# Optimization experiments

Hardware: AMD Instinct MI355X
Metric: run time of the kernel (lower is better)

The kernel has to match this reference:

```python
import jax, jax.numpy as jnp
import numpy as np

B = 128          # number of trees
DEPTH = 8        # complete binary tree depth -> 2^8-1 nodes per tree
NPT = 2 ** DEPTH - 1          # 255 nodes per tree
N = B * NPT                   # 32640 total nodes
E_T = NPT - 1                 # 254 edges per tree
F_IN = 64
H = 256


def _build_trees():
    """Complete binary trees; children of local node i are 2i+1, 2i+2."""
    idx = np.arange(NPT)
    depth = np.floor(np.log2(idx + 1)).astype(np.int64)
    order = (DEPTH - 1) - depth                 # leaves=0, root=DEPTH-1
    internal = idx[: NPT // 2]                  # nodes that have children
    parents = np.repeat(internal, 2)
    children = np.empty_like(parents)
    children[0::2] = 2 * internal + 1
    children[1::2] = 2 * internal + 2
    adj_local = np.stack([parents, children], axis=1)        # [E_T, 2]
    offs = (np.arange(B) * NPT)[:, None, None]
    adjacency = (adj_local[None, :, :] + offs).reshape(-1, 2)  # [B*E_T, 2]
    node_order = np.tile(order, B)                             # [N]
    edge_order = np.tile(order[parents], B)                    # [B*E_T]
    return node_order, adjacency, edge_order


def setup_inputs() -> dict:
    key = jax.random.key(0)
    ks = jax.random.split(key, 8)
    node_order, adjacency_list, edge_order = _build_trees()
    s = lambda k, shape, fan: jax.random.normal(k, shape, jnp.float32) * (fan ** -0.5)
    return {
        "features": jax.random.normal(ks[0], (N, F_IN), jnp.float32),
        "node_order": jnp.asarray(node_order, jnp.int32),
        "adjacency_list": jnp.asarray(adjacency_list, jnp.int32),
        "edge_order": jnp.asarray(edge_order, jnp.int32),
        "W_iou_w": s(ks[1], (3 * H, F_IN), F_IN),
        "W_iou_b": jnp.zeros((3 * H,), jnp.float32),
        "U_iou_w": s(ks[2], (3 * H, H), H),
        "W_f_w": s(ks[3], (H, F_IN), F_IN),
        "W_f_b": jnp.zeros((H,), jnp.float32),
        "U_f_w": s(ks[4], (H, H), H),
        "lin0_w": s(ks[5], (H, H), H),
        "lin0_b": jnp.zeros((H,), jnp.float32),
        "lin1_w": s(ks[6], (1, H), H),
        "lin1_b": jnp.zeros((1,), jnp.float32),
    }


def reference(features, node_order, adjacency_list, edge_order,
              W_iou_w, W_iou_b, U_iou_w, W_f_w, W_f_b, U_f_w,
              lin0_w, lin0_b, lin1_w, lin1_b):
    n = features.shape[0]
    parent = adjacency_list[:, 0]
    child = adjacency_list[:, 1]
    # input->gate projections, computed once for all nodes
    wx_iou = features @ W_iou_w.T + W_iou_b      # [N, 3H]
    wx_f = features @ W_f_w.T + W_f_b            # [N, H]
    h = jnp.zeros((n, H), features.dtype)
    c = jnp.zeros((n, H), features.dtype)
    # sequential bottom-up sweep over topological levels (static DEPTH levels)
    for t in range(DEPTH):
        nmask = (node_order == t)[:, None]
        emask = (edge_order == t).astype(features.dtype)[:, None]
        child_h = h[child]                       # [E, H] gather
        h_sum = jax.ops.segment_sum(child_h * emask, parent, num_segments=n)
        iou = wx_iou + h_sum @ U_iou_w.T         # [N, 3H]; h_sum==0 at level 0
        i, o, u = jnp.split(iou, 3, axis=1)
        i = jax.nn.sigmoid(i); o = jax.nn.sigmoid(o); u = jnp.tanh(u)
        f = jax.nn.sigmoid(wx_f[parent] + child_h @ U_f_w.T)  # [E, H]
        c_sum = jax.ops.segment_sum(f * c[child] * emask, parent, num_segments=n)
        new_c = i * u + c_sum
        new_h = o * jnp.tanh(new_c)
        h = jnp.where(nmask, new_h, h)
        c = jnp.where(nmask, new_c, c)
    # unbatch + mean-pool per tree (use_root=False); equal-size trees -> reshape
    x = h.reshape(B, NPT, H).mean(axis=1)        # [B, H]
    # MLP head: Linear -> ReLU -> (dropout inactive in eval) -> Linear
    x = x @ lin0_w.T + lin0_b
    x = jax.nn.relu(x)
    x = x @ lin1_w.T + lin1_b                    # [B, 1]
    return x.reshape(-1)                         # flattened, aux output is None
```

## Files before the change

### kernel.cpp

```cpp
#include <hip/hip_runtime.h>

#define B_TREES 128
#define NPT 255
#define NTOT (B_TREES * NPT)
#define FIN 64
#define HH 256

typedef short bf16x8 __attribute__((ext_vector_type(8)));
typedef float f32x4  __attribute__((ext_vector_type(4)));
typedef unsigned short u16;

__device__ __forceinline__ float sigf(float x) {
    return __frcp_rn(1.0f + __expf(-x));
}
__device__ __forceinline__ float tanh_fast(float x) {
    return __builtin_fmaf(2.0f, sigf(2.0f * x), -1.0f);
}
__device__ __forceinline__ u16 bf_hi(float v) {
    unsigned u = __float_as_uint(v);
    return (u16)((u + 0x7FFFu + ((u >> 16) & 1u)) >> 16);
}
__device__ __forceinline__ float bf_f(u16 b) { return __uint_as_float(((unsigned)b) << 16); }

__global__ __launch_bounds__(256) void pack_B(
    const float* __restrict__ Uiou, const float* __restrict__ Uf,
    const float* __restrict__ Wiou, const float* __restrict__ Wf,
    u16* __restrict__ Bhi, u16* __restrict__ Blo)
{
    int idx = blockIdx.x * 256 + threadIdx.x;
    int j    = idx & 7;
    int lane = (idx >> 3) & 63;
    int ksl  = (idx >> 9) % 10;
    int ct   = idx / 5120;
    int s = ct % 5, hb = ct / 5;
    int n = lane & 15, q = lane >> 4;
    int jH = hb * 16 + n;
    int k = (s < 4 ? ksl * 32 : 320 + ksl * 32) + q * 8 + j;

    float v = 0.0f;
    if (s == 4) {
        if (k < 576) v = Uf[(size_t)jH * HH + (k - 320)];
    } else {
        if (k < 256) {
            v = (s < 3) ? Uiou[(size_t)(s * 256 + jH) * HH + k]
                        : Uf[(size_t)jH * HH + k];
        } else {
            int kw = k - 256;
            v = (s < 3) ? Wiou[(size_t)(s * 256 + jH) * FIN + kw]
                        : 2.0f * Wf[(size_t)jH * FIN + kw];
        }
    }
    u16 hi = bf_hi(v);
    u16 lo = bf_hi(v - bf_f(hi));
    Bhi[idx] = hi;
    Blo[idx] = lo;
}

template<int NCT, bool LEAF>
__global__ __launch_bounds__(256, 2) void level_mfma(
    const float* __restrict__ feat,
    const u16* __restrict__ Bhi, const u16* __restrict__ Blo,
    const float* __restrict__ biou, const float* __restrict__ bfv,
    float* __restrict__ h, float* __restrict__ c,
    int Lt, int lg)
{
    constexpr int CSPLIT = 20 / NCT;
    constexpr int SUBS = NCT / 5;
    __shared__ char smem[73728];
    short* Ahi = (short*)smem;
    short* Alo = (short*)(smem + 36864);

    const int tid = threadIdx.x;
    const int lane = tid & 63, w = tid >> 6;
    const int cs = blockIdx.x % CSPLIT;
    const int rb = blockIdx.x / CSPLIT;
    const int m0 = rb * 32;
    const int msk = (1 << lg) - 1;
    const int ctbase = cs * 4 * NCT + w * NCT;

    const float4* Hf4 = (const float4*)h;
    const float4* Ff4 = (const float4*)feat;

    if constexpr (!LEAF) {
        for (int rep = 0; rep < 8; ++rep) {
            int flat = rep * 256 + tid;
            int m = flat >> 6, f4 = flat & 63;
            int mg = m0 + m;
            int b = mg >> lg, ii = Lt + (mg & msk);
            int gc = b * NPT + 2 * ii + 1;
            float4 h1 = Hf4[(size_t)gc * 64 + f4];
            float4 h2 = Hf4[(size_t)(gc + 1) * 64 + f4];
            float hsv[4] = {h1.x + h2.x, h1.y + h2.y, h1.z + h2.z, h1.w + h2.w};
            float hdv[4] = {h1.x - h2.x, h1.y - h2.y, h1.z - h2.z, h1.w - h2.w};
            int rt = m >> 4, lm = m & 15;
            int ks = f4 >> 3;
            int lane_ = lm + 16 * ((f4 >> 1) & 3);
            int j0 = (f4 & 1) * 4;
            ushort4 sh, sl, dh, dl;
            u16* shp = (u16*)&sh; u16* slp = (u16*)&sl;
            u16* dhp = (u16*)&dh; u16* dlp = (u16*)&dl;
#pragma unroll
            for (int e = 0; e < 4; ++e) {
                u16 a = bf_hi(hsv[e]); shp[e] = a; slp[e] = bf_hi(hsv[e] - bf_f(a));
                u16 d = bf_hi(hdv[e]); dhp[e] = d; dlp[e] = bf_hi(hdv[e] - bf_f(d));
            }
            int base_s = ((rt * 18 + ks) * 64 + lane_) * 8 + j0;
            int base_d = ((rt * 18 + ks + 10) * 64 + lane_) * 8 + j0;
            *(ushort4*)&Ahi[base_s] = sh;  *(ushort4*)&Alo[base_s] = sl;
            *(ushort4*)&Ahi[base_d] = dh;  *(ushort4*)&Alo[base_d] = dl;
        }
    }
    for (int rep = 0; rep < 2; ++rep) {
        int flat = rep * 256 + tid;
        int m = flat >> 4, f4 = flat & 15;
        int mg = m0 + m;
        int b = mg >> lg, ii = Lt + (mg & msk);
        int g = b * NPT + ii;
        float4 x4 = Ff4[(size_t)g * 16 + f4];
        float xv[4] = {x4.x, x4.y, x4.z, x4.w};
        int rt = m >> 4, lm = m & 15;
        int ks = 8 + (f4 >> 3);
        int lane_ = lm + 16 * ((f4 >> 1) & 3);
        int j0 = (f4 & 1) * 4;
        ushort4 xh, xl;
        u16* xhp = (u16*)&xh; u16* xlp = (u16*)&xl;
#pragma unroll
        for (int e = 0; e < 4; ++e) {
            u16 a = bf_hi(xv[e]); xhp[e] = a; xlp[e] = bf_hi(xv[e] - bf_f(a));
        }
        int base = ((rt * 18 + ks) * 64 + lane_) * 8 + j0;
        *(ushort4*)&Ahi[base] = xh;  *(ushort4*)&Alo[base] = xl;
    }
    __syncthreads();

    f32x4 acc[2][NCT];
#pragma unroll
    for (int rt = 0; rt < 2; ++rt)
#pragma unroll
        for (int i = 0; i < NCT; ++i) acc[rt][i] = (f32x4){0.f, 0.f, 0.f, 0.f};

    const int G0 = LEAF ? 8 : 0;
    for (int G = G0; G < 10; ++G) {
        bf16x8 ah[2], al[2];
#pragma unroll
        for (int rt = 0; rt < 2; ++rt) {
            ah[rt] = *(const bf16x8*)&Ahi[((rt * 18 + G) * 64 + lane) * 8];
            al[rt] = *(const bf16x8*)&Alo[((rt * 18 + G) * 64 + lane) * 8];
        }
#pragma unroll
        for (int ctl = 0; ctl < NCT; ++ctl) {
            if (ctl % 5 == 4) continue;
            size_t slot = (size_t)((ctbase + ctl) * 10 + G) * 512 + lane * 8;
            bf16x8 bh = *(const bf16x8*)(Bhi + slot);
            bf16x8 bl = *(const bf16x8*)(Blo + slot);
#pragma unroll
            for (int rt = 0; rt < 2; ++rt) {
                acc[rt][ctl] = __builtin_amdgcn_mfma_f32_16x16x32_bf16(ah[rt], bh, acc[rt][ctl], 0, 0, 0);
                acc[rt][ctl] = __builtin_amdgcn_mfma_f32_16x16x32_bf16(ah[rt], bl, acc[rt][ctl], 0, 0, 0);
                acc[rt][ctl] = __builtin_amdgcn_mfma_f32_16x16x32_bf16(al[rt], bh, acc[rt][ctl], 0, 0, 0);
            }
        }
    }
    if constexpr (!LEAF) {
        for (int G = 10; G < 18; ++G) {
            bf16x8 ah[2], al[2];
#pragma unroll
            for (int rt = 0; rt < 2; ++rt) {
                ah[rt] = *(const bf16x8*)&Ahi[((rt * 18 + G) * 64 + lane) * 8];
                al[rt] = *(const bf16x8*)&Alo[((rt * 18 + G) * 64 + lane) * 8];
            }
#pragma unroll
            for (int ctl = 4; ctl < NCT; ctl += 5) {
                size_t slot = (size_t)((ctbase + ctl) * 10 + (G - 10)) * 512 + lane * 8;
                bf16x8 bh = *(const bf16x8*)(Bhi + slot);
                bf16x8 bl = *(const bf16x8*)(Blo + slot);
#pragma unroll
                for (int rt = 0; rt < 2; ++rt) {
                    acc[rt][ctl] = __builtin_amdgcn_mfma_f32_16x16x32_bf16(ah[rt], bh, acc[rt][ctl], 0, 0, 0);
                    acc[rt][ctl] = __builtin_amdgcn_mfma_f32_16x16x32_bf16(ah[rt], bl, acc[rt][ctl], 0, 0, 0);
                    acc[rt][ctl] = __builtin_amdgcn_mfma_f32_16x16x32_bf16(al[rt], bh, acc[rt][ctl], 0, 0, 0);
                }
            }
        }
    }
    __syncthreads();

    float* sc = (float*)smem + w * 2592;
    const int n = lane & 15, q = lane >> 4;
#pragma unroll
    for (int sub = 0; sub < SUBS; ++sub) {
#pragma unroll
        for (int rt = 0; rt < 2; ++rt)
#pragma unroll
            for (int s = 0; s < 5; ++s) {
                f32x4 v = acc[rt][sub * 5 + s];
#pragma unroll
                for (int r = 0; r < 4; ++r)
                    sc[(rt * 16 + q * 4 + r) * 81 + s * 16 + n] = v[r];
            }
        int hb_abs = ctbase / 5 + sub;
        int jHb = hb_abs * 16;
        for (int it = 0; it < 8; ++it) {
            int idx = it * 64 + lane;
            int m = idx >> 4, jl = idx & 15;
            int jH = jHb + jl;
            float Ci  = sc[m * 81 + jl];
            float Co  = sc[m * 81 + 16 + jl];
            float Cu  = sc[m * 81 + 32 + jl];
            float Cfs = sc[m * 81 + 48 + jl];
            float Cfd = sc[m * 81 + 64 + jl];
            int mg = m0 + m;
            int b = mg >> lg, ii = Lt + (mg & msk);
            size_t g = (size_t)b * NPT + ii;
            float iv = sigf(Ci + biou[jH]);
            float ov = sigf(Co + biou[256 + jH]);
            float uv = tanh_fast(Cu + biou[512 + jH]);
            float cv;
            if constexpr (LEAF) {
                cv = iv * uv;
            } else {
                size_t gc = g + ii + 1;
                float bF = bfv[jH];
                float f1 = sigf(0.5f * (Cfs + Cfd) + bF);
                float f2 = sigf(0.5f * (Cfs - Cfd) + bF);
                cv = iv * uv + f1 * c[gc * HH + jH] + f2 * c[(gc + 1) * HH + jH];
            }
            float hv = ov * tanh_fast(cv);
            c[g * HH + jH] = cv;
            h[g * HH + jH] = hv;
        }
    }
}

__global__ __launch_bounds__(1024) void head_wide(
    const float* __restrict__ h,
    const float* __restrict__ l0w, const float* __restrict__ l0b,
    const float* __restrict__ l1w, const float* __restrict__ l1b,
    float* __restrict__ out)
{
    __shared__ float ms[4][HH];
    __shared__ float part[4][HH];
    __shared__ float red[4];
    int b = blockIdx.x, tid = threadIdx.x;
    int j = tid & 255, g = tid >> 8;
    const float* hb = h + (size_t)b * NPT * HH;

    float a = 0.f;
    for (int i = g; i < NPT; i += 4) a += hb[(size_t)i * HH + j];
    ms[g][j] = a;
    __syncthreads();
    if (g == 0) ms[0][j] = (ms[0][j] + ms[1][j] + ms[2][j] + ms[3][j]) * (1.0f / (float)NPT);
    __syncthreads();

    const float4* L0 = (const float4*)(l0w + (size_t)j * HH);
    float y = 0.f;
    for (int k4 = 16 * g; k4 < 16 * (g + 1); ++k4) {
        float4 wv = L0[k4];
        float4 m4 = ((const float4*)ms[0])[k4];
        y += wv.x * m4.x + wv.y * m4.y + wv.z * m4.z + wv.w * m4.w;
    }
    part[g][j] = y;
    __syncthreads();

    if (g == 0) {
        float yy = part[0][j] + part[1][j] + part[2][j] + part[3][j] + l0b[j];
        yy = fmaxf(yy, 0.f);
        float v = yy * l1w[j];
        for (int off = 32; off > 0; off >>= 1) v += __shfl_down(v, off, 64);
        if ((j & 63) == 0) red[j >> 6] = v;
    }
    __syncthreads();
    if (tid == 0) out[b] = red[0] + red[1] + red[2] + red[3] + l1b[0];
}

extern "C" void kernel_launch(void* const* d_in, const int* in_sizes, int n_in,
                              void* d_out, int out_size, void* d_ws, size_t ws_size,
                              hipStream_t stream)
{
    const float* feat = (const float*)d_in[0];
    const float* Wiou = (const float*)d_in[4];
    const float* biou = (const float*)d_in[5];
    const float* Uiou = (const float*)d_in[6];
    const float* Wf   = (const float*)d_in[7];
    const float* bfv  = (const float*)d_in[8];
    const float* Uf   = (const float*)d_in[9];
    const float* l0w  = (const float*)d_in[10];
    const float* l0b  = (const float*)d_in[11];
    const float* l1w  = (const float*)d_in[12];
    const float* l1b  = (const float*)d_in[13];

    float* h = (float*)d_ws;
    float* c = h + (size_t)NTOT * HH;
    u16* Bhi = (u16*)(c + (size_t)NTOT * HH);
    u16* Blo = Bhi + 409600;

    pack_B<<<1600, 256, 0, stream>>>(Uiou, Uf, Wiou, Wf, Bhi, Blo);

    level_mfma<10, true><<<1024, 256, 0, stream>>>(feat, Bhi, Blo, biou, bfv, h, c, 127, 7);
    level_mfma<10, false><<<512, 256, 0, stream>>>(feat, Bhi, Blo, biou, bfv, h, c, 63, 6);
    level_mfma<5, false><<<512, 256, 0, stream>>>(feat, Bhi, Blo, biou, bfv, h, c, 31, 5);
    level_mfma<5, false><<<256, 256, 0, stream>>>(feat, Bhi, Blo, biou, bfv, h, c, 15, 4);
    level_mfma<5, false><<<128, 256, 0, stream>>>(feat, Bhi, Blo, biou, bfv, h, c, 7, 3);
    level_mfma<5, false><<<64, 256, 0, stream>>>(feat, Bhi, Blo, biou, bfv, h, c, 3, 2);
    level_mfma<5, false><<<32, 256, 0, stream>>>(feat, Bhi, Blo, biou, bfv, h, c, 1, 1);
    level_mfma<5, false><<<16, 256, 0, stream>>>(feat, Bhi, Blo, biou, bfv, h, c, 0, 0);

    head_wide<<<B_TREES, 1024, 0, stream>>>(h, l0w, l0b, l1w, l1b, (float*)d_out);
}
```

Baseline: 280.8 us.

## Replace leaf-level MFMA path with FP32 FMA kernel and split mean-pool head

The leaf level, which only needs the x@W_iou projection with no child state, moves from the split-bf16 MFMA kernel into a dedicated FP32 kernel. That kernel uses a transposed W_iou layout prepared in pack_B and processes 16 nodes per block from shared memory, so the leaf path avoids the bf16 hi/lo packing. The LEAF template branch is removed from level_mfma. The per-tree mean pool is split into a 1024-block partial-sum kernel plus a final MLP kernel, giving more parallelism than 128 blocks of 1024 threads, at the cost of one extra launch.

```diff
diff --git a/kernel.cpp b/kernel.cpp
--- a/kernel.cpp
+++ b/kernel.cpp
@@ -25,38 +25,89 @@
 __global__ __launch_bounds__(256) void pack_B(
     const float* __restrict__ Uiou, const float* __restrict__ Uf,
     const float* __restrict__ Wiou, const float* __restrict__ Wf,
-    u16* __restrict__ Bhi, u16* __restrict__ Blo)
+    u16* __restrict__ Bhi, u16* __restrict__ Blo, float* __restrict__ WxT)
 {
     int idx = blockIdx.x * 256 + threadIdx.x;
-    int j    = idx & 7;
-    int lane = (idx >> 3) & 63;
-    int ksl  = (idx >> 9) % 10;
-    int ct   = idx / 5120;
-    int s = ct % 5, hb = ct / 5;
-    int n = lane & 15, q = lane >> 4;
-    int jH = hb * 16 + n;
-    int k = (s < 4 ? ksl * 32 : 320 + ksl * 32) + q * 8 + j;
-
-    float v = 0.0f;
-    if (s == 4) {
-        if (k < 576) v = Uf[(size_t)jH * HH + (k - 320)];
+    if (idx < 409600) {
+        int j    = idx & 7;
+        int lane = (idx >> 3) & 63;
+        int ksl  = (idx >> 9) % 10;
+        int ct   = idx / 5120;
+        int s = ct % 5, hb = ct / 5;
+        int n = lane & 15, q = lane >> 4;
+        int jH = hb * 16 + n;
+        int k = (s < 4 ? ksl * 32 : 320 + ksl * 32) + q * 8 + j;
+        float v = 0.0f;
+        if (s == 4) {
+            if (k < 576) v = Uf[(size_t)jH * HH + (k - 320)];
+        } else {
+            if (k < 256) {
+                v = (s < 3) ? Uiou[(size_t)(s * 256 + jH) * HH + k]
+                            : Uf[(size_t)jH * HH + k];
+            } else {
+                int kw = k - 256;
+                v = (s < 3) ? Wiou[(size_t)(s * 256 + jH) * FIN + kw]
+                            : 2.0f * Wf[(size_t)jH * FIN + kw];
+            }
+        }
+        u16 hi = bf_hi(v);
+        u16 lo = bf_hi(v - bf_f(hi));
+        Bhi[idx] = hi;
+        Blo[idx] = lo;
     } else {
-        if (k < 256) {
-            v = (s < 3) ? Uiou[(size_t)(s * 256 + jH) * HH + k]
-                        : Uf[(size_t)jH * HH + k];
-        } else {
-            int kw = k - 256;
-            v = (s < 3) ? Wiou[(size_t)(s * 256 + jH) * FIN + kw]
-                        : 2.0f * Wf[(size_t)jH * FIN + kw];
-        }
-    }
-    u16 hi = bf_hi(v);
-    u16 lo = bf_hi(v - bf_f(hi));
-    Bhi[idx] = hi;
-    Blo[idx] = lo;
-}
-
-template<int NCT, bool LEAF>
+        int idx2 = idx - 409600;
+        int k = idx2 >> 10, j = idx2 & 1023;
+        float v = (j < 768) ? Wiou[(size_t)j * 64 + k] : 2.0f * Wf[(size_t)(j - 768) * 64 + k];
+        WxT[(size_t)(k >> 2) * 4096 + j * 4 + (k & 3)] = v;
+    }
+}
+
+__global__ __launch_bounds__(256) void leaf_v2(
+    const float* __restrict__ feat,
+    const float* __restrict__ WxT, const float* __restrict__ biou,
+    float* __restrict__ h, float* __restrict__ c)
+{
+    const int NB = 16;
+    __shared__ float xs[NB][FIN];
+    int tid = threadIdx.x;
+    int l0 = blockIdx.x * NB;
+    int b = l0 >> 7;
+    int g0 = b * NPT + 127 + (l0 & 127);
+    const float* fb = feat + (size_t)g0 * FIN;
+    for (int i = tid; i < NB * FIN; i += 256) ((float*)xs)[i] = fb[i];
+    __syncthreads();
+
+    float ai[NB], ao[NB], au[NB];
+#pragma unroll
+    for (int n = 0; n < NB; ++n) { ai[n] = 0.f; ao[n] = 0.f; au[n] = 0.f; }
+
+    const float4* WxT4 = (const float4*)WxT;
+    for (int k4 = 0; k4 < 16; ++k4) {
+        size_t base = (size_t)k4 * 1024 + tid;
+        float4 wi = WxT4[base], wo = WxT4[base + 256], wu = WxT4[base + 512];
+#pragma unroll
+        for (int n = 0; n < NB; ++n) {
+            float4 x4 = ((const float4*)xs[n])[k4];
+            ai[n] += wi.x * x4.x + wi.y * x4.y + wi.z * x4.z + wi.w * x4.w;
+            ao[n] += wo.x * x4.x + wo.y * x4.y + wo.z * x4.z + wo.w * x4.w;
+            au[n] += wu.x * x4.x + wu.y * x4.y + wu.z * x4.z + wu.w * x4.w;
+        }
+    }
+
+    float bi = biou[tid], bo = biou[tid + 256], bu = biou[tid + 512];
+#pragma unroll
+    for (int n = 0; n < NB; ++n) {
+        float iv = sigf(ai[n] + bi);
+        float ov = sigf(ao[n] + bo);
+        float uv = tanh_fast(au[n] + bu);
+        float cv = iv * uv;
+        float hv = ov * tanh_fast(cv);
+        c[(size_t)(g0 + n) * HH + tid] = cv;
+        h[(size_t)(g0 + n) * HH + tid] = hv;
+    }
+}
+
+template<int NCT>
 __global__ __launch_bounds__(256, 2) void level_mfma(
     const float* __restrict__ feat,
     const u16* __restrict__ Bhi, const u16* __restrict__ Blo,
@@ -81,34 +132,32 @@
     const float4* Hf4 = (const float4*)h;
     const float4* Ff4 = (const float4*)feat;
 
-    if constexpr (!LEAF) {
-        for (int rep = 0; rep < 8; ++rep) {
-            int flat = rep * 256 + tid;
-            int m = flat >> 6, f4 = flat & 63;
-            int mg = m0 + m;
-            int b = mg >> lg, ii = Lt + (mg & msk);
-            int gc = b * NPT + 2 * ii + 1;
-            float4 h1 = Hf4[(size_t)gc * 64 + f4];
-            float4 h2 = Hf4[(size_t)(gc + 1) * 64 + f4];
-            float hsv[4] = {h1.x + h2.x, h1.y + h2.y, h1.z + h2.z, h1.w + h2.w};
-            float hdv[4] = {h1.x - h2.x, h1.y - h2.y, h1.z - h2.z, h1.w - h2.w};
-            int rt = m >> 4, lm = m & 15;
-            int ks = f4 >> 3;
-            int lane_ = lm + 16 * ((f4 >> 1) & 3);
-            int j0 = (f4 & 1) * 4;
-            ushort4 sh, sl, dh, dl;
-            u16* shp = (u16*)&sh; u16* slp = (u16*)&sl;
-            u16* dhp = (u16*)&dh; u16* dlp = (u16*)&dl;
-#pragma unroll
-            for (int e = 0; e < 4; ++e) {
-                u16 a = bf_hi(hsv[e]); shp[e] = a; slp[e] = bf_hi(hsv[e] - bf_f(a));
-                u16 d = bf_hi(hdv[e]); dhp[e] = d; dlp[e] = bf_hi(hdv[e] - bf_f(d));
-            }
-            int base_s = ((rt * 18 + ks) * 64 + lane_) * 8 + j0;
-            int base_d = ((rt * 18 + ks + 10) * 64 + lane_) * 8 + j0;
-            *(ushort4*)&Ahi[base_s] = sh;  *(ushort4*)&Alo[base_s] = sl;
-            *(ushort4*)&Ahi[base_d] = dh;  *(ushort4*)&Alo[base_d] = dl;
-        }
+    for (int rep = 0; rep < 8; ++rep) {
+        int flat = rep * 256 + tid;
+        int m = flat >> 6, f4 = flat & 63;
+        int mg = m0 + m;
+        int b = mg >> lg, ii = Lt + (mg & msk);
+        int gc = b * NPT + 2 * ii + 1;
+        float4 h1 = Hf4[(size_t)gc * 64 + f4];
+        float4 h2 = Hf4[(size_t)(gc + 1) * 64 + f4];
+        float hsv[4] = {h1.x + h2.x, h1.y + h2.y, h1.z + h2.z, h1.w + h2.w};
+        float hdv[4] = {h1.x - h2.x, h1.y - h2.y, h1.z - h2.z, h1.w - h2.w};
+        int rt = m >> 4, lm = m & 15;
+        int ks = f4 >> 3;
+        int lane_ = lm + 16 * ((f4 >> 1) & 3);
+        int j0 = (f4 & 1) * 4;
+        ushort4 sh, sl, dh, dl;
+        u16* shp = (u16*)&sh; u16* slp = (u16*)&sl;
+        u16* dhp = (u16*)&dh; u16* dlp = (u16*)&dl;
+#pragma unroll
+        for (int e = 0; e < 4; ++e) {
+            u16 a = bf_hi(hsv[e]); shp[e] = a; slp[e] = bf_hi(hsv[e] - bf_f(a));
+            u16 d = bf_hi(hdv[e]); dhp[e] = d; dlp[e] = bf_hi(hdv[e] - bf_f(d));
+        }
+        int base_s = ((rt * 18 + ks) * 64 + lane_) * 8 + j0;
+        int base_d = ((rt * 18 + ks + 10) * 64 + lane_) * 8 + j0;
+        *(ushort4*)&Ahi[base_s] = sh;  *(ushort4*)&Alo[base_s] = sl;
+        *(ushort4*)&Ahi[base_d] = dh;  *(ushort4*)&Alo[base_d] = dl;
     }
     for (int rep = 0; rep < 2; ++rep) {
         int flat = rep * 256 + tid;
@@ -139,8 +188,7 @@
 #pragma unroll
         for (int i = 0; i < NCT; ++i) acc[rt][i] = (f32x4){0.f, 0.f, 0.f, 0.f};
 
-    const int G0 = LEAF ? 8 : 0;
-    for (int G = G0; G < 10; ++G) {
+    for (int G = 0; G < 10; ++G) {
         bf16x8 ah[2], al[2];
 #pragma unroll
         for (int rt = 0; rt < 2; ++rt) {
@@ -161,25 +209,23 @@
             }
         }
     }
-    if constexpr (!LEAF) {
-        for (int G = 10; G < 18; ++G) {
-            bf16x8 ah[2], al[2];
+    for (int G = 10; G < 18; ++G) {
+        bf16x8 ah[2], al[2];
+#pragma unroll
+        for (int rt = 0; rt < 2; ++rt) {
+            ah[rt] = *(const bf16x8*)&Ahi[((rt * 18 + G) * 64 + lane) * 8];
+            al[rt] = *(const bf16x8*)&Alo[((rt * 18 + G) * 64 + lane) * 8];
+        }
+#pragma unroll
+        for (int ctl = 4; ctl < NCT; ctl += 5) {
+            size_t slot = (size_t)((ctbase + ctl) * 10 + (G - 10)) * 512 + lane * 8;
+            bf16x8 bh = *(const bf16x8*)(Bhi + slot);
+            bf16x8 bl = *(const bf16x8*)(Blo + slot);
 #pragma unroll
             for (int rt = 0; rt < 2; ++rt) {
-                ah[rt] = *(const bf16x8*)&Ahi[((rt * 18 + G) * 64 + lane) * 8];
-                al[rt] = *(const bf16x8*)&Alo[((rt * 18 + G) * 64 + lane) * 8];
-            }
-#pragma unroll
-            for (int ctl = 4; ctl < NCT; ctl += 5) {
-                size_t slot = (size_t)((ctbase + ctl) * 10 + (G - 10)) * 512 + lane * 8;
-                bf16x8 bh = *(const bf16x8*)(Bhi + slot);
-                bf16x8 bl = *(const bf16x8*)(Blo + slot);
-#pragma unroll
-                for (int rt = 0; rt < 2; ++rt) {
-                    acc[rt][ctl] = __builtin_amdgcn_mfma_f32_16x16x32_bf16(ah[rt], bh, acc[rt][ctl], 0, 0, 0);
-                    acc[rt][ctl] = __builtin_amdgcn_mfma_f32_16x16x32_bf16(ah[rt], bl, acc[rt][ctl], 0, 0, 0);
-                    acc[rt][ctl] = __builtin_amdgcn_mfma_f32_16x16x32_bf16(al[rt], bh, acc[rt][ctl], 0, 0, 0);
-                }
+                acc[rt][ctl] = __builtin_amdgcn_mfma_f32_16x16x32_bf16(ah[rt], bh, acc[rt][ctl], 0, 0, 0);
+                acc[rt][ctl] = __builtin_amdgcn_mfma_f32_16x16x32_bf16(ah[rt], bl, acc[rt][ctl], 0, 0, 0);
+                acc[rt][ctl] = __builtin_amdgcn_mfma_f32_16x16x32_bf16(al[rt], bh, acc[rt][ctl], 0, 0, 0);
             }
         }
     }
@@ -215,16 +261,11 @@
             float iv = sigf(Ci + biou[jH]);
             float ov = sigf(Co + biou[256 + jH]);
             float uv = tanh_fast(Cu + biou[512 + jH]);
-            float cv;
-            if constexpr (LEAF) {
-                cv = iv * uv;
-            } else {
-                size_t gc = g + ii + 1;
-                float bF = bfv[jH];
-                float f1 = sigf(0.5f * (Cfs + Cfd) + bF);
-                float f2 = sigf(0.5f * (Cfs - Cfd) + bF);
-                cv = iv * uv + f1 * c[gc * HH + jH] + f2 * c[(gc + 1) * HH + jH];
-            }
+            size_t gc = g + ii + 1;
+            float bF = bfv[jH];
+            float f1 = sigf(0.5f * (Cfs + Cfd) + bF);
+            float f2 = sigf(0.5f * (Cfs - Cfd) + bF);
+            float cv = iv * uv + f1 * c[gc * HH + jH] + f2 * c[(gc + 1) * HH + jH];
             float hv = ov * tanh_fast(cv);
             c[g * HH + jH] = cv;
             h[g * HH + jH] = hv;
@@ -232,43 +273,52 @@
     }
 }
 
-__global__ __launch_bounds__(1024) void head_wide(
-    const float* __restrict__ h,
+__global__ __launch_bounds__(256) void head_partial(
+    const float* __restrict__ h, float* __restrict__ hp)
+{
+    int blk = blockIdx.x;
+    int b = blk >> 3, p = blk & 7, tid = threadIdx.x;
+    const float* hb = h + ((size_t)b * NPT + p * 32) * HH;
+    int rows = (p == 7) ? 31 : 32;
+    float a0 = 0.f, a1 = 0.f, a2 = 0.f, a3 = 0.f;
+    int i = 0;
+    for (; i + 3 < rows; i += 4) {
+        a0 += hb[(size_t)(i + 0) * HH + tid];
+        a1 += hb[(size_t)(i + 1) * HH + tid];
+        a2 += hb[(size_t)(i + 2) * HH + tid];
+        a3 += hb[(size_t)(i + 3) * HH + tid];
+    }
+    for (; i < rows; ++i) a0 += hb[(size_t)i * HH + tid];
+    hp[(size_t)blk * HH + tid] = a0 + a1 + a2 + a3;
+}
+
+__global__ __launch_bounds__(256) void head_final(
+    const float* __restrict__ hp,
     const float* __restrict__ l0w, const float* __restrict__ l0b,
     const float* __restrict__ l1w, const float* __restrict__ l1b,
     float* __restrict__ out)
 {
-    __shared__ float ms[4][HH];
-    __shared__ float part[4][HH];
+    __shared__ float ms[HH];
     __shared__ float red[4];
     int b = blockIdx.x, tid = threadIdx.x;
-    int j = tid & 255, g = tid >> 8;
-    const float* hb = h + (size_t)b * NPT * HH;
-
     float a = 0.f;
-    for (int i = g; i < NPT; i += 4) a += hb[(size_t)i * HH + j];
-    ms[g][j] = a;
-    __syncthreads();
-    if (g == 0) ms[0][j] = (ms[0][j] + ms[1][j] + ms[2][j] + ms[3][j]) * (1.0f / (float)NPT);
-    __syncthreads();
-
-    const float4* L0 = (const float4*)(l0w + (size_t)j * HH);
+#pragma unroll
+    for (int p = 0; p < 8; ++p) a += hp[(size_t)(b * 8 + p) * HH + tid];
+    ms[tid] = a * (1.0f / (float)NPT);
+    __syncthreads();
+
+    const float4* L0 = (const float4*)(l0w + (size_t)tid * HH);
     float y = 0.f;
-    for (int k4 = 16 * g; k4 < 16 * (g + 1); ++k4) {
+    for (int k4 = 0; k4 < 64; ++k4) {
         float4 wv = L0[k4];
-        float4 m4 = ((const float4*)ms[0])[k4];
+        float4 m4 = ((const float4*)ms)[k4];
         y += wv.x * m4.x + wv.y * m4.y + wv.z * m4.z + wv.w * m4.w;
     }
-    part[g][j] = y;
-    __syncthreads();
-
-    if (g == 0) {
-        float yy = part[0][j] + part[1][j] + part[2][j] + part[3][j] + l0b[j];
-        yy = fmaxf(yy, 0.f);
-        float v = yy * l1w[j];
-        for (int off = 32; off > 0; off >>= 1) v += __shfl_down(v, off, 64);
-        if ((j & 63) == 0) red[j >> 6] = v;
-    }
+    y += l0b[tid];
+    y = fmaxf(y, 0.f);
+    float v = y * l1w[tid];
+    for (int off = 32; off > 0; off >>= 1) v += __shfl_down(v, off, 64);
+    if ((tid & 63) == 0) red[tid >> 6] = v;
     __syncthreads();
     if (tid == 0) out[b] = red[0] + red[1] + red[2] + red[3] + l1b[0];
 }
@@ -289,21 +339,24 @@
     const float* l1w  = (const float*)d_in[12];
     const float* l1b  = (const float*)d_in[13];
 
-    float* h = (float*)d_ws;
-    float* c = h + (size_t)NTOT * HH;
-    u16* Bhi = (u16*)(c + (size_t)NTOT * HH);
-    u16* Blo = Bhi + 409600;
-
-    pack_B<<<1600, 256, 0, stream>>>(Uiou, Uf, Wiou, Wf, Bhi, Blo);
-
-    level_mfma<10, true><<<1024, 256, 0, stream>>>(feat, Bhi, Blo, biou, bfv, h, c, 127, 7);
-    level_mfma<10, false><<<512, 256, 0, stream>>>(feat, Bhi, Blo, biou, bfv, h, c, 63, 6);
-    level_mfma<5, false><<<512, 256, 0, stream>>>(feat, Bhi, Blo, biou, bfv, h, c, 31, 5);
-    level_mfma<5, false><<<256, 256, 0, stream>>>(feat, Bhi, Blo, biou, bfv, h, c, 15, 4);
-    level_mfma<5, false><<<128, 256, 0, stream>>>(feat, Bhi, Blo, biou, bfv, h, c, 7, 3);
-    level_mfma<5, false><<<64, 256, 0, stream>>>(feat, Bhi, Blo, biou, bfv, h, c, 3, 2);
-    level_mfma<5, false><<<32, 256, 0, stream>>>(feat, Bhi, Blo, biou, bfv, h, c, 1, 1);
-    level_mfma<5, false><<<16, 256, 0, stream>>>(feat, Bhi, Blo, biou, bfv, h, c, 0, 0);
-
-    head_wide<<<B_TREES, 1024, 0, stream>>>(h, l0w, l0b, l1w, l1b, (float*)d_out);
-}
+    float* h  = (float*)d_ws;
+    float* c  = h + (size_t)NTOT * HH;
+    u16* Bhi  = (u16*)(c + (size_t)NTOT * HH);
+    u16* Blo  = Bhi + 409600;
+    float* WxT = (float*)(Blo + 409600);
+    float* hp  = WxT + 65536;
+
+    pack_B<<<1856, 256, 0, stream>>>(Uiou, Uf, Wiou, Wf, Bhi, Blo, WxT);
+
+    leaf_v2<<<1024, 256, 0, stream>>>(feat, WxT, biou, h, c);
+    level_mfma<10><<<512, 256, 0, stream>>>(feat, Bhi, Blo, biou, bfv, h, c, 63, 6);
+    level_mfma<5><<<512, 256, 0, stream>>>(feat, Bhi, Blo, biou, bfv, h, c, 31, 5);
+    level_mfma<5><<<256, 256, 0, stream>>>(feat, Bhi, Blo, biou, bfv, h, c, 15, 4);
+    level_mfma<5><<<128, 256, 0, stream>>>(feat, Bhi, Blo, biou, bfv, h, c, 7, 3);
+    level_mfma<5><<<64, 256, 0, stream>>>(feat, Bhi, Blo, biou, bfv, h, c, 3, 2);
+    level_mfma<5><<<32, 256, 0, stream>>>(feat, Bhi, Blo, biou, bfv, h, c, 1, 1);
+    level_mfma<5><<<16, 256, 0, stream>>>(feat, Bhi, Blo, biou, bfv, h, c, 0, 0);
+
+    head_partial<<<1024, 256, 0, stream>>>(h, hp);
+    head_final<<<B_TREES, 256, 0, stream>>>(hp, l0w, l0b, l1w, l1b, (float*)d_out);
+}
```

After: 297.6 us. +6.0%, slower.
